# Kernel optimization log

Measured on AMD Instinct MI355X. Metric: run time of the kernel, lower is better.

## Reference

```python
import jax, jax.numpy as jnp
import numpy as np

B, S, H = 32, 512, 1024


def setup_inputs() -> dict:
    key = jax.random.key(0)
    ks = jax.random.split(key, 8)
    scale = 1.0 / np.sqrt(H)
    x = jax.random.normal(ks[0], (B, S, H), dtype=jnp.float32)
    # realistic padding: each sequence has a valid length in [S//2, S]; 1 = masked
    lengths = jax.random.randint(ks[1], (B,), S // 2, S + 1)
    padding_mask = (jnp.arange(S)[None, :] >= lengths[:, None]).astype(jnp.float32)
    def w(k, shape):
        return (jax.random.normal(k, shape, dtype=jnp.float32) * scale).astype(jnp.float32)
    W_fw = w(ks[2], (H, 4 * H))
    U_fw = w(ks[3], (H, 4 * H))
    b_fw = jnp.zeros((4 * H,), jnp.float32)
    W_bw = w(ks[4], (H, 4 * H))
    U_bw = w(ks[5], (H, 4 * H))
    b_bw = jnp.zeros((4 * H,), jnp.float32)
    return {"src_token_embeddings": x, "padding_mask": padding_mask,
            "W_fw": W_fw, "U_fw": U_fw, "b_fw": b_fw,
            "W_bw": W_bw, "U_bw": U_bw, "b_bw": b_bw}


def _lstm_dir(x, mask, W, U, b):
    """Masked LSTM over time (Keras semantics: masked steps carry state and
    repeat the previous output). x: [B,S,H], mask: [B,S] with 1 = keep."""
    Bx, Sx, Hx = x.shape
    xz = jnp.einsum('bsh,hg->bsg', x, W) + b          # [B,S,4H] precomputed input gates
    xz_t = jnp.transpose(xz, (1, 0, 2))               # [S,B,4H]
    m_t = jnp.transpose(mask, (1, 0))[:, :, None]     # [S,B,1]
    h0 = jnp.zeros((Bx, Hx), x.dtype)

    def step(carry, inp):
        h, c, out_prev = carry
        z, m = inp
        z = z + h @ U                                  # [B,4H]
        i, f, g, o = jnp.split(z, 4, axis=-1)
        i = jax.nn.sigmoid(i)
        f = jax.nn.sigmoid(f)
        g = jnp.tanh(g)
        o = jax.nn.sigmoid(o)
        c_new = f * c + i * g
        h_new = o * jnp.tanh(c_new)
        h2 = m * h_new + (1.0 - m) * h
        c2 = m * c_new + (1.0 - m) * c
        out = m * h_new + (1.0 - m) * out_prev
        return (h2, c2, out), out

    (hT, cT, _), outs = jax.lax.scan(step, (h0, h0, h0), (xz_t, m_t))
    return jnp.transpose(outs, (1, 0, 2)), hT, cT


def reference(src_token_embeddings, padding_mask, W_fw, U_fw, b_fw, W_bw, U_bw, b_bw):
    x = src_token_embeddings
    mask = 1.0 - padding_mask                          # 1 = keep, as in the Keras call
    out_fw, h_fw, c_fw = _lstm_dir(x, mask, W_fw, U_fw, b_fw)
    # backward direction: process time-reversed sequence, then reverse outputs back
    out_bw_rev, h_bw, c_bw = _lstm_dir(x[:, ::-1], mask[:, ::-1], W_bw, U_bw, b_bw)
    out_bw = out_bw_rev[:, ::-1]
    encoder_outputs = jnp.concatenate([out_fw, out_bw], axis=-1)  # [B,S,2H]
    return encoder_outputs, h_fw, c_fw, h_bw, c_bw
```

## Files before the change

kernel.cpp:

```cpp
#include <hip/hip_runtime.h>
#include <hip/hip_bf16.h>

#define B 32
#define S 512
#define H 1024
#define G 4096
#define NBLK 256
#define HSLOT 65536

typedef __attribute__((ext_vector_type(8))) short bf16x8;
typedef __attribute__((ext_vector_type(8))) unsigned short u16x8;
typedef __attribute__((ext_vector_type(4))) float f32x4;

__device__ __forceinline__ unsigned short f2bf(float v) {
    __hip_bfloat16 b = __float2bfloat16(v);
    return *reinterpret_cast<unsigned short*>(&b);
}
__device__ __forceinline__ float bf2f(unsigned short u) {
    union { float f; unsigned int i; } v; v.i = ((unsigned int)u) << 16; return v.f;
}
#define MFMA(a, b, c) __builtin_amdgcn_mfma_f32_16x16x32_bf16(a, b, c, 0, 0, 0)
#define ALOAD(p)    __hip_atomic_load((p),  __ATOMIC_RELAXED, __HIP_MEMORY_SCOPE_AGENT)
#define ASTORE(p,v) __hip_atomic_store((p), (v), __ATOMIC_RELAXED, __HIP_MEMORY_SCOPE_AGENT)

__global__ __launch_bounds__(256)
void prep_weights(const float* __restrict__ fw, const float* __restrict__ bw,
                  unsigned short* __restrict__ dst)
{
    size_t idx = (size_t)blockIdx.x * 256 + threadIdx.x;
    int lane = idx & 63;
    int f    = (idx >> 6) & 15;
    int w    = (idx >> 10) & 3;
    int blk  = (int)(idx >> 12);
    int dir  = blk >> 7, jg = blk & 127;
    int ks = f >> 1, ct = f & 1;

    int c  = ct * 16 + (lane & 15);
    int g  = (c >> 3) * H + jg * 8 + (c & 7);
    int kk = w * 256 + ks * 32 + ((lane >> 4) * 8);

    const float* src = dir ? bw : fw;
    u16x8 o;
#pragma unroll
    for (int i = 0; i < 8; ++i)
        o[i] = f2bf(src[(size_t)(kk + i) * G + g]);
    *(u16x8*)&dst[idx * 8] = o;
}

__global__ __launch_bounds__(256)
void prep_x(const float* __restrict__ x, unsigned short* __restrict__ xbf)
{
    size_t i8 = ((size_t)blockIdx.x * 256 + threadIdx.x) * 8;
    float4 v0 = *(const float4*)&x[i8];
    float4 v1 = *(const float4*)&x[i8 + 4];
    u16x8 o;
    o[0] = f2bf(v0.x); o[1] = f2bf(v0.y); o[2] = f2bf(v0.z); o[3] = f2bf(v0.w);
    o[4] = f2bf(v1.x); o[5] = f2bf(v1.y); o[6] = f2bf(v1.z); o[7] = f2bf(v1.w);
    *(u16x8*)&xbf[i8] = o;
}

__global__ __launch_bounds__(512, 1)
void lstm_persist(const unsigned short* __restrict__ wbufU,
                  const unsigned short* __restrict__ wbufW,
                  const unsigned short* __restrict__ xbf,
                  unsigned short* __restrict__ hhist,
                  unsigned int* __restrict__ mbox,
                  const float* __restrict__ pad,
                  const float* __restrict__ bfw, const float* __restrict__ bbw,
                  float* __restrict__ dout)
{
    const int blk = blockIdx.x;
    const int dir = blk >> 7;
    const int jg  = blk & 127;
    const int j0  = jg * 8;
    const int tid = threadIdx.x;
    const int wave = tid >> 6;
    const int lane = tid & 63;

    __shared__ short Uw[32768];
    __shared__ float red[4][2][16][33];
    __shared__ unsigned short ring[8][32][36];
    __shared__ unsigned rcnt;
    __shared__ unsigned gcnt;
    __shared__ int ring_ready[8];

    if (tid == 0) { rcnt = 0; gcnt = 0; }
    if (tid < 8) ring_ready[tid] = 0;
    __syncthreads();

    const int arow  = lane & 15;
    const int akoff = (lane >> 4) * 8;
    const int drow  = (lane >> 4) * 4;
    const int dcol  = lane & 15;
    const float* bsrc = dir ? bbw : bfw;
    const float wb0 = bsrc[(dcol >> 3) * H + j0 + (dcol & 7)];
    const float wb1 = bsrc[(((16 + dcol) >> 3)) * H + j0 + ((16 + dcol) & 7)];

    if (wave < 4) {
        {
            const unsigned short* src = wbufU + (((size_t)blk * 4 + wave) * 16) * 512 + lane * 8;
#pragma unroll
            for (int f = 0; f < 16; ++f)
                *(u16x8*)&Uw[((wave * 16 + f) * 64 + lane) * 8] = *(const u16x8*)(src + f * 512);
        }

        float hst = 0.f, cst = 0.f;
        const int gb  = (tid >> 3) & 31;
        const int gj  = tid & 7;
        const int gbt = gb >> 4, grow = gb & 15;
        const f32x4 zero4 = {0.f, 0.f, 0.f, 0.f};
        const unsigned* mb_in = mbox + ((size_t)(dir * 128) + jg) * 128 + wave * 32;
        unsigned int* mb_out = mbox + ((size_t)(dir * 128) + wave * 32) * 128 + jg;

        for (int t = 0; t < S; ++t) {
            const int s = dir ? (S - 1 - t) : t;
            float pv = pad[gb * S + s];

            if (t) {
                bool ok;
                do {
                    unsigned v = ALOAD(&mb_in[lane & 31]);
                    ok = __all(v >= (unsigned)t);
                    if (!ok) __builtin_amdgcn_s_sleep(1);
                } while (!ok);
                asm volatile("" ::: "memory");
            }

            f32x4 u00 = zero4, u01 = zero4, u10 = zero4, u11 = zero4;
            const unsigned short* hb = hhist + (size_t)t * HSLOT
                                     + ((size_t)(dir * B) + arow) * H + wave * 256 + akoff;
#pragma unroll
            for (int ks = 0; ks < 8; ++ks) {
                bf16x8 a0 = *(const bf16x8*)(hb + ks * 32);
                bf16x8 a1 = *(const bf16x8*)(hb + 16 * H + ks * 32);
                bf16x8 b0 = *(const bf16x8*)&Uw[((wave * 16 + ks * 2 + 0) * 64 + lane) * 8];
                bf16x8 b1 = *(const bf16x8*)&Uw[((wave * 16 + ks * 2 + 1) * 64 + lane) * 8];
                u00 = MFMA(a0, b0, u00); u01 = MFMA(a0, b1, u01);
                u10 = MFMA(a1, b0, u10); u11 = MFMA(a1, b1, u11);
            }
#pragma unroll
            for (int r = 0; r < 4; ++r) {
                red[wave][0][drow + r][dcol]      = u00[r];
                red[wave][0][drow + r][16 + dcol] = u01[r];
                red[wave][1][drow + r][dcol]      = u10[r];
                red[wave][1][drow + r][16 + dcol] = u11[r];
            }
            asm volatile("s_waitcnt lgkmcnt(0)" ::: "memory");
            if (lane == 0) atomicAdd(&rcnt, 1u);
            {
                const unsigned need = 4u * (unsigned)(t + 1);
                while (*(volatile unsigned*)&rcnt < need) {}
                asm volatile("" ::: "memory");
            }

            while (*(volatile int*)&ring_ready[t & 7] < t + 1) {}
            asm volatile("" ::: "memory");

            float z[4];
#pragma unroll
            for (int q = 0; q < 4; ++q) {
                const int c = q * 8 + gj;
                float zz = bf2f(ring[t & 7][gb][c]);
#pragma unroll
                for (int w = 0; w < 4; ++w) zz += red[w][gbt][grow][c];
                z[q] = zz;
            }
            float ig = 1.f / (1.f + expf(-z[0]));
            float fg = 1.f / (1.f + expf(-z[1]));
            float gg = tanhf(z[2]);
            float og = 1.f / (1.f + expf(-z[3]));

            float m  = 1.f - pv;
            float cn = fg * cst + ig * gg;
            float hn = og * tanhf(cn);
            float h2 = fmaf(m, hn - hst, hst);
            float c2 = fmaf(m, cn - cst, cst);
            hst = h2; cst = c2;

            unsigned u = (unsigned)f2bf(h2);
            const int gl = lane & ~3;
            unsigned v0 = (unsigned)__shfl((int)u, gl + 0);
            unsigned v1 = (unsigned)__shfl((int)u, gl + 1);
            unsigned v2 = (unsigned)__shfl((int)u, gl + 2);
            unsigned v3 = (unsigned)__shfl((int)u, gl + 3);
            if ((lane & 3) == 0) {
                unsigned long long pk = (unsigned long long)(v0 & 0xffffu)
                                      | ((unsigned long long)(v1 & 0xffffu) << 16)
                                      | ((unsigned long long)(v2 & 0xffffu) << 32)
                                      | ((unsigned long long)(v3 & 0xffffu) << 48);
                unsigned long long* hp = (unsigned long long*)
                    (hhist + (size_t)(t + 1) * HSLOT
                           + ((size_t)(dir * B) + gb) * H + j0 + gj);
                ASTORE(hp, pk);
            }
            asm volatile("s_waitcnt vmcnt(0)" ::: "memory");
            if (lane == 0) atomicAdd(&gcnt, 1u);
            {
                const unsigned need = 4u * (unsigned)(t + 1);
                while (*(volatile unsigned*)&gcnt < need) {}
                asm volatile("" ::: "memory");
                if (lane < 32)
                    ASTORE(mb_out + (size_t)lane * 128, (unsigned)(t + 1));
            }

            __builtin_nontemporal_store(h2,
                &dout[((size_t)gb * S + s) * (2 * H) + dir * H + j0 + gj]);
            if (t == S - 1) {
                size_t base = (size_t)B * S * 2 * H;
                __builtin_nontemporal_store(h2,
                    &dout[base + dir * 2 * B * H + gb * H + j0 + gj]);
                __builtin_nontemporal_store(c2,
                    &dout[base + dir * 2 * B * H + B * H + gb * H + j0 + gj]);
            }
        }
    } else {
        const f32x4 zero4 = {0.f, 0.f, 0.f, 0.f};
        for (int fs = wave - 4; fs < S; fs += 4) {
            if (fs >= 8) {
                const unsigned need = 4u * (unsigned)(fs - 7);
                while (*(volatile unsigned*)&gcnt < need)
                    __builtin_amdgcn_s_sleep(2);
                asm volatile("" ::: "memory");
            }
            const int s2 = dir ? (S - 1 - fs) : fs;
            f32x4 a00 = zero4, a01 = zero4, a10 = zero4, a11 = zero4;
            for (int sl = 0; sl < 4; ++sl) {
                const unsigned short* wbase =
                    wbufW + (((size_t)blk * 4 + sl) * 16) * 512 + lane * 8;
                bf16x8 wf[16];
#pragma unroll
                for (int f = 0; f < 16; ++f) wf[f] = *(const bf16x8*)(wbase + f * 512);
                const unsigned short* A0 =
                    xbf + ((size_t)arow * S + s2) * H + sl * 256 + akoff;
#pragma unroll
                for (int ks = 0; ks < 8; ++ks) {
                    bf16x8 x0 = *(const bf16x8*)(A0 + ks * 32);
                    bf16x8 x1 = *(const bf16x8*)(A0 + (size_t)16 * S * H + ks * 32);
                    a00 = MFMA(x0, wf[ks*2+0], a00); a01 = MFMA(x0, wf[ks*2+1], a01);
                    a10 = MFMA(x1, wf[ks*2+0], a10); a11 = MFMA(x1, wf[ks*2+1], a11);
                }
            }
            const int slot = fs & 7;
#pragma unroll
            for (int r = 0; r < 4; ++r) {
                ring[slot][drow + r][dcol]           = f2bf(a00[r] + wb0);
                ring[slot][drow + r][16 + dcol]      = f2bf(a01[r] + wb1);
                ring[slot][16 + drow + r][dcol]      = f2bf(a10[r] + wb0);
                ring[slot][16 + drow + r][16 + dcol] = f2bf(a11[r] + wb1);
            }
            asm volatile("s_waitcnt lgkmcnt(0)" ::: "memory");
            if (lane == 0) *(volatile int*)&ring_ready[slot] = fs + 1;
        }
    }
}

extern "C" void kernel_launch(void* const* d_in, const int* in_sizes, int n_in,
                              void* d_out, int out_size, void* d_ws, size_t ws_size,
                              hipStream_t stream)
{
    const float* x   = (const float*)d_in[0];
    const float* pad = (const float*)d_in[1];
    const float* Wfw = (const float*)d_in[2];
    const float* Ufw = (const float*)d_in[3];
    const float* bfw = (const float*)d_in[4];
    const float* Wbw = (const float*)d_in[5];
    const float* Ubw = (const float*)d_in[6];
    const float* bbw = (const float*)d_in[7];
    float* out = (float*)d_out;

    char* w = (char*)d_ws;
    unsigned short* wbufW = (unsigned short*)w;
    unsigned short* wbufU = wbufW + (size_t)1048576 * 8;
    unsigned short* xbf   = wbufU + (size_t)1048576 * 8;
    unsigned short* hhist = xbf + (size_t)B * S * H;
    unsigned int*   mbox  = (unsigned int*)(hhist + (size_t)(S + 1) * HSLOT);

    hipMemsetAsync(hhist, 0, (size_t)HSLOT * sizeof(unsigned short), stream);
    hipMemsetAsync(mbox, 0, (size_t)2 * 128 * 128 * sizeof(unsigned int), stream);

    prep_x<<<8192, 256, 0, stream>>>(x, xbf);
    prep_weights<<<4096, 256, 0, stream>>>(Wfw, Wbw, wbufW);
    prep_weights<<<4096, 256, 0, stream>>>(Ufw, Ubw, wbufU);

    void* args[] = { (void*)&wbufU, (void*)&wbufW, (void*)&xbf, (void*)&hhist,
                     (void*)&mbox, (void*)&pad,
                     (void*)&bfw, (void*)&bbw, (void*)&out };
    hipLaunchCooperativeKernel((void*)lstm_persist, dim3(NBLK), dim3(512),
                               args, 0, stream);
}
```

Measured before the change: 3.120 ms.

## Replace mailbox flag handshake with sentinel-polled hidden-state data

Removes the per-step mailbox counters between blocks. Consumers now spin directly on the 64-bit packed hidden-state words in the history buffer until none equals an all-ones sentinel. The history buffer is pre-filled with 0xFF each call. Producers no longer wait for store completion, run an intra-block barrier or publish flags, which takes a global round trip off each recurrent step. The cost is a large 0xFF memset every call and more polling traffic. A real h value that packs to all-ones would be mistaken for the sentinel.

```diff
diff --git a/kernel.cpp b/kernel.cpp
--- a/kernel.cpp
+++ b/kernel.cpp
@@ -64,7 +64,6 @@
                   const unsigned short* __restrict__ wbufW,
                   const unsigned short* __restrict__ xbf,
                   unsigned short* __restrict__ hhist,
-                  unsigned int* __restrict__ mbox,
                   const float* __restrict__ pad,
                   const float* __restrict__ bfw, const float* __restrict__ bbw,
                   float* __restrict__ dout)
@@ -109,34 +108,44 @@
         const int gj  = tid & 7;
         const int gbt = gb >> 4, grow = gb & 15;
         const f32x4 zero4 = {0.f, 0.f, 0.f, 0.f};
-        const unsigned* mb_in = mbox + ((size_t)(dir * 128) + jg) * 128 + wave * 32;
-        unsigned int* mb_out = mbox + ((size_t)(dir * 128) + wave * 32) * 128 + jg;
+        const unsigned long long SENT = ~0ull;
 
         for (int t = 0; t < S; ++t) {
             const int s = dir ? (S - 1 - t) : t;
             float pv = pad[gb * S + s];
 
-            if (t) {
-                bool ok;
-                do {
-                    unsigned v = ALOAD(&mb_in[lane & 31]);
-                    ok = __all(v >= (unsigned)t);
-                    if (!ok) __builtin_amdgcn_s_sleep(1);
-                } while (!ok);
-                asm volatile("" ::: "memory");
+            const unsigned long long* hb64 = (const unsigned long long*)
+                (hhist + (size_t)t * HSLOT
+                       + ((size_t)(dir * B) + arow) * H + wave * 256 + akoff);
+            const unsigned long long* hb64b = hb64 + 4 * H;
+            unsigned long long v[32];
+            unsigned missing = 0xffffffffu;
+            for (;;) {
+#pragma unroll
+                for (int i = 0; i < 16; ++i) {
+                    if (missing & (1u << i))
+                        v[i] = ALOAD(hb64 + (i >> 1) * 8 + (i & 1));
+                    if (missing & (1u << (16 + i)))
+                        v[16 + i] = ALOAD(hb64b + (i >> 1) * 8 + (i & 1));
+                }
+#pragma unroll
+                for (int i = 0; i < 32; ++i)
+                    if ((missing & (1u << i)) && v[i] != SENT)
+                        missing &= ~(1u << i);
+                if (!__any((int)(missing != 0u))) break;
+                __builtin_amdgcn_s_sleep(1);
             }
 
             f32x4 u00 = zero4, u01 = zero4, u10 = zero4, u11 = zero4;
-            const unsigned short* hb = hhist + (size_t)t * HSLOT
-                                     + ((size_t)(dir * B) + arow) * H + wave * 256 + akoff;
 #pragma unroll
             for (int ks = 0; ks < 8; ++ks) {
-                bf16x8 a0 = *(const bf16x8*)(hb + ks * 32);
-                bf16x8 a1 = *(const bf16x8*)(hb + 16 * H + ks * 32);
+                union { unsigned long long q[2]; bf16x8 x; } ua0, ua1;
+                ua0.q[0] = v[2 * ks];      ua0.q[1] = v[2 * ks + 1];
+                ua1.q[0] = v[16 + 2 * ks]; ua1.q[1] = v[16 + 2 * ks + 1];
                 bf16x8 b0 = *(const bf16x8*)&Uw[((wave * 16 + ks * 2 + 0) * 64 + lane) * 8];
                 bf16x8 b1 = *(const bf16x8*)&Uw[((wave * 16 + ks * 2 + 1) * 64 + lane) * 8];
-                u00 = MFMA(a0, b0, u00); u01 = MFMA(a0, b1, u01);
-                u10 = MFMA(a1, b0, u10); u11 = MFMA(a1, b1, u11);
+                u00 = MFMA(ua0.x, b0, u00); u01 = MFMA(ua0.x, b1, u01);
+                u10 = MFMA(ua1.x, b0, u10); u11 = MFMA(ua1.x, b1, u11);
             }
 #pragma unroll
             for (int r = 0; r < 4; ++r) {
@@ -165,6 +174,9 @@
                 for (int w = 0; w < 4; ++w) zz += red[w][gbt][grow][c];
                 z[q] = zz;
             }
+            asm volatile("s_waitcnt lgkmcnt(0)" ::: "memory");
+            if (lane == 0) atomicAdd(&gcnt, 1u);
+
             float ig = 1.f / (1.f + expf(-z[0]));
             float fg = 1.f / (1.f + expf(-z[1]));
             float gg = tanhf(z[2]);
@@ -193,15 +205,6 @@
                            + ((size_t)(dir * B) + gb) * H + j0 + gj);
                 ASTORE(hp, pk);
             }
-            asm volatile("s_waitcnt vmcnt(0)" ::: "memory");
-            if (lane == 0) atomicAdd(&gcnt, 1u);
-            {
-                const unsigned need = 4u * (unsigned)(t + 1);
-                while (*(volatile unsigned*)&gcnt < need) {}
-                asm volatile("" ::: "memory");
-                if (lane < 32)
-                    ASTORE(mb_out + (size_t)lane * 128, (unsigned)(t + 1));
-            }
 
             __builtin_nontemporal_store(h2,
                 &dout[((size_t)gb * S + s) * (2 * H) + dir * H + j0 + gj]);
@@ -273,18 +276,17 @@
     unsigned short* wbufU = wbufW + (size_t)1048576 * 8;
     unsigned short* xbf   = wbufU + (size_t)1048576 * 8;
     unsigned short* hhist = xbf + (size_t)B * S * H;
-    unsigned int*   mbox  = (unsigned int*)(hhist + (size_t)(S + 1) * HSLOT);
-
-    hipMemsetAsync(hhist, 0, (size_t)HSLOT * sizeof(unsigned short), stream);
-    hipMemsetAsync(mbox, 0, (size_t)2 * 128 * 128 * sizeof(unsigned int), stream);
+
+    hipMemsetAsync(hhist, 0x00, (size_t)HSLOT * sizeof(unsigned short), stream);
+    hipMemsetAsync(hhist + (size_t)HSLOT, 0xFF,
+                   (size_t)S * HSLOT * sizeof(unsigned short), stream);
 
     prep_x<<<8192, 256, 0, stream>>>(x, xbf);
     prep_weights<<<4096, 256, 0, stream>>>(Wfw, Wbw, wbufW);
     prep_weights<<<4096, 256, 0, stream>>>(Ufw, Ubw, wbufU);
 
     void* args[] = { (void*)&wbufU, (void*)&wbufW, (void*)&xbf, (void*)&hhist,
-                     (void*)&mbox, (void*)&pad,
-                     (void*)&bfw, (void*)&bbw, (void*)&out };
+                     (void*)&pad, (void*)&bfw, (void*)&bbw, (void*)&out };
     hipLaunchCooperativeKernel((void*)lstm_persist, dim3(NBLK), dim3(512),
                                args, 0, stream);
 }
```

After: 4.794 ms. +53.6%, slower.
